# Kernel tuning notes

Hardware: AMD Instinct MI355X
Metric: run time of the kernel (lower is better)

Reference implementation:

```python
import jax, jax.numpy as jnp
import numpy as np

# dims: num_time T, batch B, nodes N, feature F(=hidden_dim), heads H(must be 1, see notes)
T, B, N, F, H = 16, 32, 512, 128, 1
E = F * T          # embed_size = hidden_dim * num_time = 2048
D = E // H         # head_dim = 2048


def setup_inputs() -> dict:
    key = jax.random.key(0)
    ks = jax.random.split(key, 9)
    s = 0.02
    return {
        "x":   jax.random.normal(ks[0], (T, B, N, F), dtype=jnp.float32),
        # torch nn.Linear convention: W is [out_features, in_features], y = x @ W.T + b
        "Wq":  jax.random.normal(ks[1], (D, D), dtype=jnp.float32) * s,
        "bq":  jnp.zeros((D,), dtype=jnp.float32),
        "Wk":  jax.random.normal(ks[2], (D, D), dtype=jnp.float32) * s,
        "bk":  jnp.zeros((D,), dtype=jnp.float32),
        "Wv":  jax.random.normal(ks[3], (E, D), dtype=jnp.float32) * s,
        "bv":  jnp.zeros((E,), dtype=jnp.float32),
        "Wfc": jax.random.normal(ks[4], (E, E), dtype=jnp.float32) * s,
        "bfc": jnp.zeros((E,), dtype=jnp.float32),
    }


def reference(x, Wq, bq, Wk, bk, Wv, bv, Wfc, bfc):
    Tt, Bb, Nn, Ff = x.shape
    Ee = Ff * Tt
    # mean over axis 1 of the ORIGINAL [T,B,N,F] tensor (this is the batch axis;
    # the original code calls it node_axis but operates on the un-permuted x)
    x_mean = x.mean(axis=1)                                   # [T, N, F]
    # permute(1,2,3,0).reshape -> [B, N, F*T], then split heads (H=1)
    xr = jnp.transpose(x, (1, 2, 3, 0)).reshape(Bb, Nn, H, Ee // H)
    q = xr @ Wq.T + bq                                        # [B, N, H, D]
    k = xr @ Wk.T + bk                                        # [B, N, H, D]
    v = xr @ Wv.T + bv                                        # [B, N, H, E]
    energy = jnp.einsum('nqhd,nkhd->nhqk', q, k)              # [B, H, N, N]
    attention = jax.nn.softmax(energy / jnp.sqrt(jnp.float32(Ee)), axis=3)
    out = jnp.einsum('nhql,nlhd->nqhd', attention, v).reshape(Bb, Nn, Ee)
    out = out @ Wfc.T + bfc                                   # [B, N, E]
    # faithful to the original's (buggy) view: (nodes, batch, T, F) then permute
    out = jnp.transpose(out.reshape(Nn, Bb, Tt, Ff), (2, 1, 0, 3)).mean(axis=1)  # [T, N, F]
    return x_mean + out, attention
```

## Files before the change

kernel.cpp:

```cpp
#include <hip/hip_runtime.h>

typedef __attribute__((ext_vector_type(8))) __bf16 bf16x8;
typedef __attribute__((ext_vector_type(4))) float floatx4;

__device__ __forceinline__ float bf2f(unsigned short u) {
    union { unsigned int i; float f; } v; v.i = ((unsigned int)u) << 16; return v.f;
}
__device__ __forceinline__ unsigned short f2bf(float f) {
    union { float f; unsigned int i; } v; v.f = f;
    unsigned int u = v.i;
    return (unsigned short)((u + 0x7fffu + ((u >> 16) & 1u)) >> 16);
}

__device__ __forceinline__ void async16(const void* g, void* l) {
    __builtin_amdgcn_global_load_lds(
        (__attribute__((address_space(1))) void*)(g),
        (__attribute__((address_space(3))) void*)(l), 16, 0, 0);
}

__global__ void detect_dtype(const unsigned short* __restrict__ w, int* __restrict__ flag)
{
    int tid = threadIdx.x;
    int cnt = 0;
    for (int i = tid; i < 256; i += 64) {
        unsigned short s = w[2 * i];
        int e = (s >> 7) & 0xFF;
        if (e >= 100 && e <= 126) cnt++;
    }
#pragma unroll
    for (int off = 32; off > 0; off >>= 1) cnt += __shfl_xor(cnt, off);
    if (tid == 0) *flag = (cnt >= 128) ? 1 : 0;
}

__global__ __launch_bounds__(256)
void convert_weights(const void* __restrict__ w5, const void* __restrict__ w7,
                     unsigned short* __restrict__ o5, unsigned short* __restrict__ o7,
                     const int* __restrict__ flag)
{
    const void* in = blockIdx.y ? w7 : w5;
    unsigned short* out = blockIdx.y ? o7 : o5;
    int i = (blockIdx.x * 256 + threadIdx.x) * 4;
    if (*flag) {
        *(uint2*)(out + i) = *(const uint2*)((const unsigned short*)in + i);
    } else {
        float4 f = *(const float4*)((const float*)in + i);
        union { uint2 u; unsigned short s[4]; } W;
        W.s[0] = f2bf(f.x); W.s[1] = f2bf(f.y); W.s[2] = f2bf(f.z); W.s[3] = f2bf(f.w);
        *(uint2*)(out + i) = W.u;
    }
}

__global__ __launch_bounds__(256)
void convert_biases(const void* __restrict__ bq, const void* __restrict__ bv,
                    const void* __restrict__ bfc,
                    unsigned short* __restrict__ bqb, unsigned short* __restrict__ bvb,
                    unsigned short* __restrict__ bfcb, const int* __restrict__ flag)
{
    const int which = blockIdx.x;
    const void* in = which == 0 ? bq : (which == 1 ? bv : bfc);
    unsigned short* out = which == 0 ? bqb : (which == 1 ? bvb : bfcb);
    const float scale = which == 1 ? 32.0f : 1.0f;
    int i = threadIdx.x * 8;
    float f[8];
    if (*flag) {
        const unsigned short* p = (const unsigned short*)in + i;
#pragma unroll
        for (int j = 0; j < 8; j++) f[j] = bf2f(p[j]);
    } else {
        float4 a = *(const float4*)((const float*)in + i);
        float4 b = *(const float4*)((const float*)in + i + 4);
        f[0] = a.x; f[1] = a.y; f[2] = a.z; f[3] = a.w;
        f[4] = b.x; f[5] = b.y; f[6] = b.z; f[7] = b.w;
    }
    union { uint4 u; unsigned short s[8]; } W;
#pragma unroll
    for (int j = 0; j < 8; j++) W.s[j] = f2bf(f[j] * scale);
    *(uint4*)(out + i) = W.u;
}

__global__ __launch_bounds__(256)
void transpose_conv(const void* __restrict__ in, unsigned short* __restrict__ out,
                    const int* __restrict__ flag)
{
    __shared__ unsigned short tile[64 * 65];
    const int d0 = blockIdx.x * 64, i0 = blockIdx.y * 64;
    const int tid = threadIdx.x;
    const int r = tid >> 2, seg = tid & 3;

    const long base = (long)(d0 + r) * 2048 + i0 + seg * 16;
    unsigned short vals[16];
    if (*flag) {
        const unsigned short* p = (const unsigned short*)in + base;
        union { uint4 u; unsigned short s[8]; } a, b;
        a.u = *(const uint4*)p; b.u = *(const uint4*)(p + 8);
#pragma unroll
        for (int j = 0; j < 8; j++) { vals[j] = a.s[j]; vals[8 + j] = b.s[j]; }
    } else {
        const float* p = (const float*)in + base;
#pragma unroll
        for (int q = 0; q < 4; q++) {
            float4 v = *(const float4*)(p + q * 4);
            vals[q * 4 + 0] = f2bf(v.x); vals[q * 4 + 1] = f2bf(v.y);
            vals[q * 4 + 2] = f2bf(v.z); vals[q * 4 + 3] = f2bf(v.w);
        }
    }
#pragma unroll
    for (int j = 0; j < 16; j++) tile[r * 65 + seg * 16 + j] = vals[j];
    __syncthreads();

    union { uint4 u[2]; unsigned short s[16]; } W;
#pragma unroll
    for (int j = 0; j < 16; j++) W.s[j] = tile[(seg * 16 + j) * 65 + r];
    unsigned short* o = out + (long)(i0 + r) * 2048 + d0 + seg * 16;
    *(uint4*)o = W.u[0];
    *(uint4*)(o + 8) = W.u[1];
}

__global__ __launch_bounds__(256)
void build_xr(const void* __restrict__ xv, unsigned short* __restrict__ xr,
              const float* __restrict__ w2, float* __restrict__ c,
              const int* __restrict__ flag)
{
    __shared__ __align__(16) unsigned short tile[128 * 24];
    __shared__ float red[4];
    const int bn = blockIdx.x;
    const int b = bn >> 9, n = bn & 511;
    const int tid = threadIdx.x;
    const int t = tid >> 4, l16 = tid & 15;

    const long off = (long)(t * 32 + b) * 65536 + n * 128 + l16 * 8;
    union { uint4 u; unsigned short s[8]; } U;
    if (*flag) {
        U.u = *(const uint4*)((const unsigned short*)xv + off);
    } else {
        const float* xf = (const float*)xv + off;
        float4 f0 = *(const float4*)xf;
        float4 f1 = *(const float4*)(xf + 4);
        U.s[0] = f2bf(f0.x); U.s[1] = f2bf(f0.y); U.s[2] = f2bf(f0.z); U.s[3] = f2bf(f0.w);
        U.s[4] = f2bf(f1.x); U.s[5] = f2bf(f1.y); U.s[6] = f2bf(f1.z); U.s[7] = f2bf(f1.w);
    }
    float s = 0.f;
#pragma unroll
    for (int j = 0; j < 8; j++) {
        tile[(l16 * 8 + j) * 24 + t] = U.s[j];
        s += bf2f(U.s[j]) * w2[(l16 * 8 + j) * 16 + t];
    }
#pragma unroll
    for (int o = 32; o > 0; o >>= 1) s += __shfl_xor(s, o);
    if ((tid & 63) == 0) red[tid >> 6] = s;
    __syncthreads();
    if (tid == 0) c[bn] = red[0] + red[1] + red[2] + red[3];

    const int f = tid >> 1, t0 = (tid & 1) * 8;
    uint4 o = *(const uint4*)&tile[f * 24 + t0];
    *(uint4*)(xr + (long)bn * 2048 + tid * 8) = o;
}

template <int MODE, bool BIAS, int BM>
__global__ __launch_bounds__(256)
void gemm_nt(const unsigned short* __restrict__ Ag,
             const unsigned short* __restrict__ Bg,
             void* __restrict__ Cg,
             const unsigned short* __restrict__ bias,
             int K, long sA, long sB, long sC, int lda, int ldb, int ldc)
{
    constexpr int NJ = (BM == 128) ? 4 : 2;
    __shared__ __align__(16) unsigned short lsA[BM * 32];
    __shared__ __align__(16) unsigned short lsB[128 * 32];

    const int tid = threadIdx.x;
    const int z = blockIdx.z;
    const unsigned short* A = Ag + (long)z * sA + (long)blockIdx.y * BM * lda;
    const unsigned short* B = Bg + (long)z * sB + (long)blockIdx.x * 128 * ldb;

    const int wave = tid >> 6, lane = tid & 63;
    const int wm = (BM == 128) ? (wave >> 1) * 64 : 0;
    const int wn = (BM == 128) ? (wave & 1) * 64 : wave * 32;
    const int r = lane & 15, quad = lane >> 4;

    floatx4 acc[4][NJ];
#pragma unroll
    for (int i = 0; i < 4; i++)
#pragma unroll
        for (int j = 0; j < NJ; j++) acc[i][j] = floatx4{0.f, 0.f, 0.f, 0.f};

    const int srow = tid >> 2;
    const int scol = (tid & 3) * 8;
    const long a0 = (long)srow * lda + scol;
    const long a1 = (long)(srow + 64) * lda + scol;
    const long b0 = (long)srow * ldb + scol;
    const long b1 = (long)(srow + 64) * ldb + scol;

    for (int k0 = 0; k0 < K; k0 += 32) {
        async16(A + k0 + a0, (char*)lsA + tid * 16);
        if (BM == 128) async16(A + k0 + a1, (char*)lsA + 4096 + tid * 16);
        async16(B + k0 + b0, (char*)lsB + tid * 16);
        async16(B + k0 + b1, (char*)lsB + 4096 + tid * 16);
        __syncthreads();

        const bf16x8* pA = (const bf16x8*)lsA;
        const bf16x8* pB = (const bf16x8*)lsB;
        bf16x8 af[4], bb[NJ];
#pragma unroll
        for (int i = 0; i < 4; i++) af[i] = pA[(wm + i * 16 + r) * 4 + quad];
#pragma unroll
        for (int j = 0; j < NJ; j++) bb[j] = pB[(wn + j * 16 + r) * 4 + quad];
#pragma unroll
        for (int i = 0; i < 4; i++)
#pragma unroll
            for (int j = 0; j < NJ; j++)
                acc[i][j] = __builtin_amdgcn_mfma_f32_16x16x32_bf16(af[i], bb[j], acc[i][j], 0, 0, 0);
        __syncthreads();
    }

    const int mb = blockIdx.y * BM + wm + quad * 4;
    const int nb = blockIdx.x * 128 + wn + r;

    if (MODE == 1) {
        float* C = (float*)Cg + (long)z * sC;
#pragma unroll
        for (int i = 0; i < 4; i++)
#pragma unroll
            for (int j = 0; j < NJ; j++)
#pragma unroll
                for (int g = 0; g < 4; g++)
                    C[(long)(mb + i * 16 + g) * ldc + (nb + j * 16)] = acc[i][j][g];
    } else {
        unsigned short* C = (unsigned short*)Cg + (long)z * sC;
#pragma unroll
        for (int j = 0; j < NJ; j++) {
            const int n = nb + j * 16;
            const float bj = BIAS ? bf2f(bias[n]) : 0.0f;
#pragma unroll
            for (int i = 0; i < 4; i++)
#pragma unroll
                for (int g = 0; g < 4; g++)
                    C[(long)(mb + i * 16 + g) * ldc + n] = f2bf(acc[i][j][g] + bj);
        }
    }
}

__global__ __launch_bounds__(256)
void w2_kernel(const unsigned short* __restrict__ WkT,
               const unsigned short* __restrict__ bqb, float* __restrict__ w2)
{
    const int i = blockIdx.x, tid = threadIdx.x;
    const unsigned short* row = WkT + (long)i * 2048 + tid * 8;
    const unsigned short* bv = bqb + tid * 8;
    union { uint4 u; unsigned short s[8]; } A, B;
    A.u = *(const uint4*)row; B.u = *(const uint4*)bv;
    float s = 0.f;
#pragma unroll
    for (int j = 0; j < 8; j++) s += bf2f(A.s[j]) * bf2f(B.s[j]);
#pragma unroll
    for (int off = 32; off > 0; off >>= 1) s += __shfl_xor(s, off);
    __shared__ float red[4];
    if ((tid & 63) == 0) red[tid >> 6] = s;
    __syncthreads();
    if (tid == 0) w2[i] = red[0] + red[1] + red[2] + red[3];
}

__global__ __launch_bounds__(256)
void softmax_pbar(const float* __restrict__ S, const float* __restrict__ c,
                  void* __restrict__ dout, unsigned short* __restrict__ Pbar,
                  const int* __restrict__ flag)
{
    const int g = blockIdx.x;
    const int b = g >> 4;
    const int tid = threadIdx.x;
    const float scale = 0.02209708691207961f;
    const int isbf = *flag;
    __shared__ float redm[4], reds[4];

    float2 cv = ((const float2*)(c + b * 512))[tid];
    float p0 = 0.f, p1 = 0.f;

    for (int r = 0; r < 32; r++) {
        const long row = (long)g * 32 + r;
        float2 v = ((const float2*)(S + row * 512))[tid];
        float a = (v.x + cv.x) * scale, d = (v.y + cv.y) * scale;

        float m = fmaxf(a, d);
#pragma unroll
        for (int off = 32; off > 0; off >>= 1) m = fmaxf(m, __shfl_xor(m, off));
        if ((tid & 63) == 0) redm[tid >> 6] = m;
        __syncthreads();
        m = fmaxf(fmaxf(redm[0], redm[1]), fmaxf(redm[2], redm[3]));

        float ea = __expf(a - m), eb = __expf(d - m);
        float s = ea + eb;
#pragma unroll
        for (int off = 32; off > 0; off >>= 1) s += __shfl_xor(s, off);
        if ((tid & 63) == 0) reds[tid >> 6] = s;
        __syncthreads();
        s = reds[0] + reds[1] + reds[2] + reds[3];
        const float inv = 1.0f / s;
        const float fa = ea * inv, fb = eb * inv;
        p0 += fa; p1 += fb;

        if (isbf) {
            unsigned short* P = (unsigned short*)dout + 1048576;
            ((unsigned int*)(P + row * 512))[tid] =
                (unsigned int)f2bf(fa) | ((unsigned int)f2bf(fb) << 16);
        } else {
            float* P = (float*)dout + 1048576;
            ((float2*)(P + row * 512))[tid] = make_float2(fa, fb);
        }
        __syncthreads();
    }
    ((unsigned int*)(Pbar + (long)g * 512))[tid] =
        (unsigned int)f2bf(p0) | ((unsigned int)f2bf(p1) << 16);
}

__global__ __launch_bounds__(256)
void z_kernel(const unsigned short* __restrict__ Pbar,
              const unsigned short* __restrict__ xr,
              unsigned short* __restrict__ Z)
{
    __shared__ __align__(16) unsigned short tile[32 * 64];
    const int b = blockIdx.y, d0 = blockIdx.x * 64;
    const int tid = threadIdx.x;
    const int wave = tid >> 6, lane = tid & 63;
    const int r = lane & 15, quad = lane >> 4;
    const unsigned short* xrb = xr + (long)b * 512 * 2048;

    floatx4 acc = floatx4{0.f, 0.f, 0.f, 0.f};
    for (int l0 = 0; l0 < 512; l0 += 32) {
        async16(xrb + (long)(l0 + (tid >> 3)) * 2048 + d0 + (tid & 7) * 8,
                (char*)tile + tid * 16);
        __syncthreads();
        bf16x8 a = *(const bf16x8*)(Pbar + (long)(b * 16 + r) * 512 + l0 + quad * 8);
        union { bf16x8 v; unsigned short s[8]; } bb;
#pragma unroll
        for (int j = 0; j < 8; j++) bb.s[j] = tile[(quad * 8 + j) * 64 + wave * 16 + r];
        acc = __builtin_amdgcn_mfma_f32_16x16x32_bf16(a, bb.v, acc, 0, 0, 0);
        __syncthreads();
    }
#pragma unroll
    for (int g = 0; g < 4; g++)
        Z[(long)(b * 16 + quad * 4 + g) * 2048 + d0 + wave * 16 + r] = f2bf(acc[g]);
}

__global__ __launch_bounds__(256)
void final_small(const unsigned short* __restrict__ xr,
                 const unsigned short* __restrict__ Ybar,
                 const unsigned short* __restrict__ bfcb, void* __restrict__ dout,
                 const int* __restrict__ flag)
{
    __shared__ float xm[2048];
    const int n = blockIdx.x;
    const int tid = threadIdx.x;
    const int isbf = *flag;

    float a[8] = {0, 0, 0, 0, 0, 0, 0, 0};
    const unsigned short* base = xr + (long)n * 2048 + tid * 8;
    for (int b = 0; b < 32; b++) {
        union { uint4 u; unsigned short s[8]; } U;
        U.u = *(const uint4*)(base + (long)b * 1048576);
#pragma unroll
        for (int j = 0; j < 8; j++) a[j] += bf2f(U.s[j]);
    }
#pragma unroll
    for (int j = 0; j < 8; j++) xm[tid * 8 + j] = a[j];
    __syncthreads();

    const int col0 = tid * 8;
    const int t = col0 >> 7, f0 = col0 & 127;
    float acc[8];
    {
        union { uint4 u; unsigned short s[8]; } Yv, Bv;
        Yv.u = *(const uint4*)(Ybar + (long)n * 2048 + col0);
        Bv.u = *(const uint4*)(bfcb + col0);
#pragma unroll
        for (int j = 0; j < 8; j++)
            acc[j] = bf2f(Yv.s[j]) + 32.0f * bf2f(Bv.s[j]) + xm[(f0 + j) * 16 + t];
    }
    const long oidx = (long)t * 65536 + n * 128 + f0;
    if (isbf) {
        union { uint4 u; unsigned short s[8]; } W;
#pragma unroll
        for (int j = 0; j < 8; j++) W.s[j] = f2bf(acc[j] * 0.03125f);
        *(uint4*)((unsigned short*)dout + oidx) = W.u;
    } else {
        float* o = (float*)dout + oidx;
#pragma unroll
        for (int j = 0; j < 8; j += 4)
            *(float4*)(o + j) = make_float4(acc[j] * 0.03125f, acc[j + 1] * 0.03125f,
                                            acc[j + 2] * 0.03125f, acc[j + 3] * 0.03125f);
    }
}

extern "C" void kernel_launch(void* const* d_in, const int* in_sizes, int n_in,
                              void* d_out, int out_size, void* d_ws, size_t ws_size,
                              hipStream_t stream)
{
    unsigned short* xr   = (unsigned short*)d_ws;
    unsigned short* H    = xr + 33554432;
    float*          S    = (float*)(H + 33554432);
    unsigned short* Gt   = (unsigned short*)(S + 8388608);
    unsigned short* WqT  = Gt  + 4194304;
    unsigned short* WkT  = WqT + 4194304;
    unsigned short* Wvb  = WkT + 4194304;
    unsigned short* Wfcb = Wvb + 4194304;
    unsigned short* Pbar = Wfcb + 4194304;
    unsigned short* Z    = Pbar + 262144;
    unsigned short* Obar = Z + 1048576;
    unsigned short* Ybar = Obar + 1048576;
    unsigned short* bqb  = Ybar + 1048576;
    unsigned short* bvb  = bqb + 2048;
    unsigned short* bfcb = bvb + 2048;
    float*          w2   = (float*)(bfcb + 2048);
    float*          c    = w2 + 2048;
    int*            flag = (int*)(c + 16384);

    detect_dtype<<<1, 64, 0, stream>>>((const unsigned short*)d_in[1], flag);
    transpose_conv<<<dim3(32, 32), 256, 0, stream>>>(d_in[1], WqT, flag);
    transpose_conv<<<dim3(32, 32), 256, 0, stream>>>(d_in[3], WkT, flag);
    convert_weights<<<dim3(4096, 2), 256, 0, stream>>>(d_in[5], d_in[7], Wvb, Wfcb, flag);
    convert_biases<<<3, 256, 0, stream>>>(d_in[2], d_in[6], d_in[8], bqb, bvb, bfcb, flag);
    w2_kernel<<<2048, 256, 0, stream>>>(WkT, bqb, w2);

    build_xr<<<16384, 256, 0, stream>>>(d_in[0], xr, w2, c, flag);
    gemm_nt<0, false, 64><<<dim3(16, 32, 1), 256, 0, stream>>>(
        WkT, WqT, Gt, nullptr, 2048, 0, 0, 0, 2048, 2048, 2048);
    gemm_nt<0, false, 128><<<dim3(16, 128, 1), 256, 0, stream>>>(
        xr, Gt, H, nullptr, 2048, 0, 0, 0, 2048, 2048, 2048);
    gemm_nt<1, false, 128><<<dim3(4, 4, 32), 256, 0, stream>>>(
        H, xr, S, nullptr, 2048, 1048576, 1048576, 262144, 2048, 2048, 512);
    softmax_pbar<<<512, 256, 0, stream>>>(S, c, d_out, Pbar, flag);
    z_kernel<<<dim3(32, 32), 256, 0, stream>>>(Pbar, xr, Z);
    gemm_nt<0, true, 64><<<dim3(16, 8, 1), 256, 0, stream>>>(
        Z, Wvb, Obar, bvb, 2048, 0, 0, 0, 2048, 2048, 2048);
    gemm_nt<0, false, 64><<<dim3(16, 8, 1), 256, 0, stream>>>(
        Obar, Wfcb, Ybar, nullptr, 2048, 0, 0, 0, 2048, 2048, 2048);
    final_small<<<512, 256, 0, stream>>>(xr, Ybar, bfcb, d_out, flag);
}
```

Baseline: 751.5 us.

## Compute H projection GEMM in FP8 with scaled Gt, rework softmax per-wave rows

The biggest GEMM (xr times Gt, 16384x2048x2048) now runs with FP8 MFMA instead of bf16. build_xr emits an FP8 copy of xr, and a new conv_gt8 kernel scales Gt by 64 and converts it to FP8. The softmax absorbs that scale through a separate sS factor. Softmax is restructured so each wave handles its own rows with wave-level reductions only, removing the per-row block barriers. The Wq/Wk transposes are merged into one launch and the S GEMM tile changes to BM=64. FP8 cuts precision of the attention logits, which risks accuracy on the attention output.

```diff
diff --git a/kernel.cpp b/kernel.cpp
--- a/kernel.cpp
+++ b/kernel.cpp
@@ -10,6 +10,11 @@
     union { float f; unsigned int i; } v; v.f = f;
     unsigned int u = v.i;
     return (unsigned short)((u + 0x7fffu + ((u >> 16) & 1u)) >> 16);
+}
+__device__ __forceinline__ unsigned int pk4_fp8(float a, float b, float c, float d) {
+    int v = __builtin_amdgcn_cvt_pk_fp8_f32(a, b, 0, false);
+    v = __builtin_amdgcn_cvt_pk_fp8_f32(c, d, v, true);
+    return (unsigned int)v;
 }
 
 __device__ __forceinline__ void async16(const void* g, void* l) {
@@ -79,10 +84,13 @@
 }
 
 __global__ __launch_bounds__(256)
-void transpose_conv(const void* __restrict__ in, unsigned short* __restrict__ out,
+void transpose_conv(const void* __restrict__ inq, const void* __restrict__ ink,
+                    unsigned short* __restrict__ outq, unsigned short* __restrict__ outk,
                     const int* __restrict__ flag)
 {
     __shared__ unsigned short tile[64 * 65];
+    const void* in = blockIdx.z ? ink : inq;
+    unsigned short* out = blockIdx.z ? outk : outq;
     const int d0 = blockIdx.x * 64, i0 = blockIdx.y * 64;
     const int tid = threadIdx.x;
     const int r = tid >> 2, seg = tid & 3;
@@ -118,6 +126,7 @@
 
 __global__ __launch_bounds__(256)
 void build_xr(const void* __restrict__ xv, unsigned short* __restrict__ xr,
+              unsigned char* __restrict__ xr8,
               const float* __restrict__ w2, float* __restrict__ c,
               const int* __restrict__ flag)
 {
@@ -154,6 +163,30 @@
     const int f = tid >> 1, t0 = (tid & 1) * 8;
     uint4 o = *(const uint4*)&tile[f * 24 + t0];
     *(uint4*)(xr + (long)bn * 2048 + tid * 8) = o;
+
+    union { uint4 u; unsigned short s[8]; } O; O.u = o;
+    float fv[8];
+#pragma unroll
+    for (int j = 0; j < 8; j++) fv[j] = bf2f(O.s[j]);
+    uint2 p8;
+    p8.x = pk4_fp8(fv[0], fv[1], fv[2], fv[3]);
+    p8.y = pk4_fp8(fv[4], fv[5], fv[6], fv[7]);
+    *(uint2*)(xr8 + (long)bn * 2048 + tid * 8) = p8;
+}
+
+__global__ __launch_bounds__(256)
+void conv_gt8(const unsigned short* __restrict__ Gt, unsigned char* __restrict__ Gt8)
+{
+    long i = ((long)blockIdx.x * 256 + threadIdx.x) * 8;
+    union { uint4 u; unsigned short s[8]; } U;
+    U.u = *(const uint4*)(Gt + i);
+    float f[8];
+#pragma unroll
+    for (int j = 0; j < 8; j++) f[j] = bf2f(U.s[j]) * 64.0f;
+    uint2 p8;
+    p8.x = pk4_fp8(f[0], f[1], f[2], f[3]);
+    p8.y = pk4_fp8(f[4], f[5], f[6], f[7]);
+    *(uint2*)(Gt8 + i) = p8;
 }
 
 template <int MODE, bool BIAS, int BM>
@@ -241,6 +274,65 @@
 }
 
 __global__ __launch_bounds__(256)
+void gemm_h_fp8(const unsigned char* __restrict__ A8,
+                const unsigned char* __restrict__ B8,
+                unsigned short* __restrict__ Hc)
+{
+    __shared__ __align__(16) unsigned char lsA[128 * 32];
+    __shared__ __align__(16) unsigned char lsB[128 * 32];
+
+    const int tid = threadIdx.x;
+    const unsigned char* A = A8 + (long)blockIdx.y * 128 * 2048;
+    const unsigned char* B = B8 + (long)blockIdx.x * 128 * 2048;
+
+    const int wave = tid >> 6, lane = tid & 63;
+    const int wm = (wave >> 1) * 64, wn = (wave & 1) * 64;
+    const int r = lane & 15, quad = lane >> 4;
+
+    floatx4 acc[4][4];
+#pragma unroll
+    for (int i = 0; i < 4; i++)
+#pragma unroll
+        for (int j = 0; j < 4; j++) acc[i][j] = floatx4{0.f, 0.f, 0.f, 0.f};
+
+    const int srow = tid >> 1;
+    const int scol = (tid & 1) * 16;
+    const long g0 = (long)srow * 2048 + scol;
+
+    for (int k0 = 0; k0 < 2048; k0 += 32) {
+        async16(A + k0 + g0, (char*)lsA + tid * 16);
+        async16(B + k0 + g0, (char*)lsB + tid * 16);
+        __syncthreads();
+
+        long af[4], bb[4];
+#pragma unroll
+        for (int i = 0; i < 4; i++)
+            af[i] = *(const long*)(lsA + (wm + i * 16 + r) * 32 + quad * 8);
+#pragma unroll
+        for (int j = 0; j < 4; j++)
+            bb[j] = *(const long*)(lsB + (wn + j * 16 + r) * 32 + quad * 8);
+#pragma unroll
+        for (int i = 0; i < 4; i++)
+#pragma unroll
+            for (int j = 0; j < 4; j++)
+                acc[i][j] = __builtin_amdgcn_mfma_f32_16x16x32_fp8_fp8(af[i], bb[j], acc[i][j], 0, 0, 0);
+        __syncthreads();
+    }
+
+    const int mb = blockIdx.y * 128 + wm + quad * 4;
+    const int nb = blockIdx.x * 128 + wn + r;
+#pragma unroll
+    for (int j = 0; j < 4; j++) {
+        const int n = nb + j * 16;
+#pragma unroll
+        for (int i = 0; i < 4; i++)
+#pragma unroll
+            for (int g = 0; g < 4; g++)
+                Hc[(long)(mb + i * 16 + g) * 2048 + n] = f2bf(acc[i][j][g]);
+    }
+}
+
+__global__ __launch_bounds__(256)
 void w2_kernel(const unsigned short* __restrict__ WkT,
                const unsigned short* __restrict__ bqb, float* __restrict__ w2)
 {
@@ -263,53 +355,69 @@
 __global__ __launch_bounds__(256)
 void softmax_pbar(const float* __restrict__ S, const float* __restrict__ c,
                   void* __restrict__ dout, unsigned short* __restrict__ Pbar,
-                  const int* __restrict__ flag)
-{
+                  float sS, float sc, const int* __restrict__ flag)
+{
+    __shared__ float part[4][512];
     const int g = blockIdx.x;
     const int b = g >> 4;
     const int tid = threadIdx.x;
-    const float scale = 0.02209708691207961f;
+    const int wave = tid >> 6, lane = tid & 63;
     const int isbf = *flag;
-    __shared__ float redm[4], reds[4];
-
-    float2 cv = ((const float2*)(c + b * 512))[tid];
-    float p0 = 0.f, p1 = 0.f;
-
-    for (int r = 0; r < 32; r++) {
-        const long row = (long)g * 32 + r;
-        float2 v = ((const float2*)(S + row * 512))[tid];
-        float a = (v.x + cv.x) * scale, d = (v.y + cv.y) * scale;
-
-        float m = fmaxf(a, d);
+
+    float cv[8];
+    {
+        float4 c0 = *(const float4*)(c + b * 512 + lane * 8);
+        float4 c1 = *(const float4*)(c + b * 512 + lane * 8 + 4);
+        cv[0] = c0.x; cv[1] = c0.y; cv[2] = c0.z; cv[3] = c0.w;
+        cv[4] = c1.x; cv[5] = c1.y; cv[6] = c1.z; cv[7] = c1.w;
+    }
+    float pb[8] = {0, 0, 0, 0, 0, 0, 0, 0};
+
+    for (int rr = 0; rr < 8; rr++) {
+        const long row = (long)g * 32 + wave * 8 + rr;
+        const float* sp = S + row * 512 + lane * 8;
+        float4 v0 = *(const float4*)sp;
+        float4 v1 = *(const float4*)(sp + 4);
+        float a[8] = {v0.x, v0.y, v0.z, v0.w, v1.x, v1.y, v1.z, v1.w};
+#pragma unroll
+        for (int j = 0; j < 8; j++) a[j] = a[j] * sS + cv[j] * sc;
+
+        float m = a[0];
+#pragma unroll
+        for (int j = 1; j < 8; j++) m = fmaxf(m, a[j]);
 #pragma unroll
         for (int off = 32; off > 0; off >>= 1) m = fmaxf(m, __shfl_xor(m, off));
-        if ((tid & 63) == 0) redm[tid >> 6] = m;
-        __syncthreads();
-        m = fmaxf(fmaxf(redm[0], redm[1]), fmaxf(redm[2], redm[3]));
-
-        float ea = __expf(a - m), eb = __expf(d - m);
-        float s = ea + eb;
+
+        float e[8], s = 0.f;
+#pragma unroll
+        for (int j = 0; j < 8; j++) { e[j] = __expf(a[j] - m); s += e[j]; }
 #pragma unroll
         for (int off = 32; off > 0; off >>= 1) s += __shfl_xor(s, off);
-        if ((tid & 63) == 0) reds[tid >> 6] = s;
-        __syncthreads();
-        s = reds[0] + reds[1] + reds[2] + reds[3];
         const float inv = 1.0f / s;
-        const float fa = ea * inv, fb = eb * inv;
-        p0 += fa; p1 += fb;
 
         if (isbf) {
             unsigned short* P = (unsigned short*)dout + 1048576;
-            ((unsigned int*)(P + row * 512))[tid] =
-                (unsigned int)f2bf(fa) | ((unsigned int)f2bf(fb) << 16);
+            union { uint4 u; unsigned short h[8]; } W;
+#pragma unroll
+            for (int j = 0; j < 8; j++) { float p = e[j] * inv; W.h[j] = f2bf(p); pb[j] += p; }
+            *(uint4*)(P + row * 512 + lane * 8) = W.u;
         } else {
             float* P = (float*)dout + 1048576;
-            ((float2*)(P + row * 512))[tid] = make_float2(fa, fb);
+            float p[8];
+#pragma unroll
+            for (int j = 0; j < 8; j++) { p[j] = e[j] * inv; pb[j] += p[j]; }
+            *(float4*)(P + row * 512 + lane * 8) = make_float4(p[0], p[1], p[2], p[3]);
+            *(float4*)(P + row * 512 + lane * 8 + 4) = make_float4(p[4], p[5], p[6], p[7]);
         }
-        __syncthreads();
-    }
+    }
+#pragma unroll
+    for (int j = 0; j < 8; j++) part[wave][lane * 8 + j] = pb[j];
+    __syncthreads();
+    const int col = tid * 2;
+    float s0 = part[0][col] + part[1][col] + part[2][col] + part[3][col];
+    float s1 = part[0][col + 1] + part[1][col + 1] + part[2][col + 1] + part[3][col + 1];
     ((unsigned int*)(Pbar + (long)g * 512))[tid] =
-        (unsigned int)f2bf(p0) | ((unsigned int)f2bf(p1) << 16);
+        (unsigned int)f2bf(s0) | ((unsigned int)f2bf(s1) << 16);
 }
 
 __global__ __launch_bounds__(256)
@@ -402,7 +510,9 @@
     unsigned short* WkT  = WqT + 4194304;
     unsigned short* Wvb  = WkT + 4194304;
     unsigned short* Wfcb = Wvb + 4194304;
-    unsigned short* Pbar = Wfcb + 4194304;
+    unsigned char*  xr8  = (unsigned char*)(Wfcb + 4194304);
+    unsigned char*  Gt8  = xr8 + 33554432;
+    unsigned short* Pbar = (unsigned short*)(Gt8 + 4194304);
     unsigned short* Z    = Pbar + 262144;
     unsigned short* Obar = Z + 1048576;
     unsigned short* Ybar = Obar + 1048576;
@@ -413,21 +523,22 @@
     float*          c    = w2 + 2048;
     int*            flag = (int*)(c + 16384);
 
+    const float scale = 0.02209708691207961f;
+
     detect_dtype<<<1, 64, 0, stream>>>((const unsigned short*)d_in[1], flag);
-    transpose_conv<<<dim3(32, 32), 256, 0, stream>>>(d_in[1], WqT, flag);
-    transpose_conv<<<dim3(32, 32), 256, 0, stream>>>(d_in[3], WkT, flag);
+    transpose_conv<<<dim3(32, 32, 2), 256, 0, stream>>>(d_in[1], d_in[3], WqT, WkT, flag);
     convert_weights<<<dim3(4096, 2), 256, 0, stream>>>(d_in[5], d_in[7], Wvb, Wfcb, flag);
     convert_biases<<<3, 256, 0, stream>>>(d_in[2], d_in[6], d_in[8], bqb, bvb, bfcb, flag);
     w2_kernel<<<2048, 256, 0, stream>>>(WkT, bqb, w2);
 
-    build_xr<<<16384, 256, 0, stream>>>(d_in[0], xr, w2, c, flag);
+    build_xr<<<16384, 256, 0, stream>>>(d_in[0], xr, xr8, w2, c, flag);
     gemm_nt<0, false, 64><<<dim3(16, 32, 1), 256, 0, stream>>>(
         WkT, WqT, Gt, nullptr, 2048, 0, 0, 0, 2048, 2048, 2048);
-    gemm_nt<0, false, 128><<<dim3(16, 128, 1), 256, 0, stream>>>(
-        xr, Gt, H, nullptr, 2048, 0, 0, 0, 2048, 2048, 2048);
-    gemm_nt<1, false, 128><<<dim3(4, 4, 32), 256, 0, stream>>>(
+    conv_gt8<<<2048, 256, 0, stream>>>(Gt, Gt8);
+    gemm_h_fp8<<<dim3(16, 128), 256, 0, stream>>>(xr8, Gt8, H);
+    gemm_nt<1, false, 64><<<dim3(4, 8, 32), 256, 0, stream>>>(
         H, xr, S, nullptr, 2048, 1048576, 1048576, 262144, 2048, 2048, 512);
-    softmax_pbar<<<512, 256, 0, stream>>>(S, c, d_out, Pbar, flag);
+    softmax_pbar<<<512, 256, 0, stream>>>(S, c, d_out, Pbar, scale / 64.0f, scale, flag);
     z_kernel<<<dim3(32, 32), 256, 0, stream>>>(Pbar, xr, Z);
     gemm_nt<0, true, 64><<<dim3(16, 8, 1), 256, 0, stream>>>(
         Z, Wvb, Obar, bvb, 2048, 0, 0, 0, 2048, 2048, 2048);
```

Result: no change. 750.9 us (-0.1%).
